# Kernel tuning notes

Measured on AMD Instinct MI355X. Metric: run time of the kernel, lower is better.

The kernel has to match this reference:

```python
import jax, jax.numpy as jnp
from jax import lax
import numpy as np

H = 48; W = 48; C_IN = 256; A_PER = 3
M = A_PER * H * W            # 6912 anchors
IMG = 768.0                  # square image, clip bound for x and y
OBJ_THR = 0.3; IOU_THR = 0.7; TOP_K = 2000
NEG = -1e9                   # finite sentinel for masked scores


def _make_anchors():
    stride = IMG / H
    base = 2.0 * stride
    ratios = np.array([0.5, 1.0, 2.0])
    ws = base * np.sqrt(ratios)          # [3]
    hs = base / np.sqrt(ratios)
    cx = (np.arange(W) + 0.5) * stride
    cy = (np.arange(H) + 0.5) * stride
    cxg, cyg = np.meshgrid(cx, cy)       # [H, W]
    anc = np.stack([
        cxg[None] - ws[:, None, None] / 2,
        cyg[None] - hs[:, None, None] / 2,
        cxg[None] + ws[:, None, None] / 2,
        cyg[None] + hs[:, None, None] / 2,
    ], axis=-1)                           # [3, H, W, 4] matches (anchor, h, w) flatten order
    return jnp.asarray(anc.reshape(-1, 4), jnp.float32)


def setup_inputs() -> dict:
    key = jax.random.key(0)
    ks = jax.random.split(key, 4)
    x = jax.random.normal(ks[0], (1, C_IN, H, W), jnp.float32)
    conv_w = jax.random.normal(ks[1], (256, 256, 3, 3), jnp.float32) * 0.02
    conv_b = jnp.zeros((256,), jnp.float32)
    det_w = jax.random.normal(ks[2], (3, 256, 1, 1), jnp.float32) * 0.02
    det_b = jnp.zeros((3,), jnp.float32)
    reg_w = jax.random.normal(ks[3], (12, 256, 1, 1), jnp.float32) * 0.02
    reg_b = jnp.zeros((12,), jnp.float32)
    anchors = _make_anchors()
    return {"x": x, "conv_w": conv_w, "conv_b": conv_b, "det_w": det_w,
            "det_b": det_b, "reg_w": reg_w, "reg_b": reg_b, "anchors": anchors}


def reference(x, conv_w, conv_b, det_w, det_b, reg_w, reg_b, anchors):
    # ---- FPN 3x3 conv + RPN head (1x1 convs) ----
    inter = lax.conv_general_dilated(
        x, conv_w, (1, 1), 'SAME',
        dimension_numbers=('NCHW', 'OIHW', 'NCHW')) + conv_b[None, :, None, None]
    obj = jax.nn.sigmoid(jnp.einsum('nchw,oc->nohw', inter, det_w[:, :, 0, 0])
                         + det_b[None, :, None, None])          # [1,3,H,W]
    reg = (jnp.einsum('nchw,oc->nohw', inter, reg_w[:, :, 0, 0])
           + reg_b[None, :, None, None])                        # [1,12,H,W]

    scores = obj.reshape(-1)                                    # [M], (anchor,h,w) order
    deltas = reg.reshape(1, 4, A_PER, H, W).transpose(0, 2, 3, 4, 1).reshape(-1, 4)

    # ---- box decode (preserves the source's cx/cy quirk: cx = y1 + w/2, cy = x1 + h/2) ----
    x1, y1, x2, y2 = anchors[:, 0], anchors[:, 1], anchors[:, 2], anchors[:, 3]
    aw = x2 - x1; ah = y2 - y1
    acx = y1 + aw / 2; acy = x1 + ah / 2
    dx, dy, dw, dh = deltas[:, 0], deltas[:, 1], deltas[:, 2], deltas[:, 3]
    px = acx + dx * aw; py = acy + dy * ah
    pw = aw * jnp.exp(dw); ph = ah * jnp.exp(dh)
    boxes = jnp.stack([px - pw / 2, py - ph / 2, px + pw / 2, py + ph / 2], axis=-1)

    # ---- clip to image ----
    boxes = jnp.clip(boxes, 0.0, IMG)

    # ---- validity: degenerate filter (source's naming quirk) + objectness threshold ----
    hts = boxes[:, 2] - boxes[:, 0]
    wds = boxes[:, 3] - boxes[:, 1]
    valid = (hts > 0) & (wds > 0) & (scores > OBJ_THR)

    # ---- greedy NMS (jit-friendly: sort, pairwise IoU, sequential suppression) ----
    s = jnp.where(valid, scores, NEG)
    order = jnp.argsort(-s)
    b = boxes[order]; v = valid[order]; ss = s[order]
    area = (b[:, 2] - b[:, 0]) * (b[:, 3] - b[:, 1])             # [M]
    iw = jnp.clip(jnp.minimum(b[:, None, 2], b[None, :, 2])
                  - jnp.maximum(b[:, None, 0], b[None, :, 0]), 0.0)
    ih = jnp.clip(jnp.minimum(b[:, None, 3], b[None, :, 3])
                  - jnp.maximum(b[:, None, 1], b[None, :, 1]), 0.0)
    inter_a = iw * ih                                             # [M,M]
    iou = inter_a / jnp.maximum(area[:, None] + area[None, :] - inter_a, 1e-9)

    idx = jnp.arange(M)

    def body(suppressed, i):
        keep_i = v[i] & (~suppressed[i])
        sup = keep_i & (iou[i] > IOU_THR) & (idx > i)
        return suppressed | sup, keep_i

    _, keeps = lax.scan(body, jnp.zeros(M, bool), idx)            # keep mask (sorted order)

    # ---- top-k proposal selection (fixed K, padded with sentinels) ----
    out_s = jnp.where(keeps, ss, NEG)
    topv, topi = lax.top_k(out_s, TOP_K)
    vtop = keeps[topi]
    out_scores = jnp.where(vtop, topv, -1.0)                      # [TOP_K]
    out_boxes = jnp.where(vtop[:, None], b[topi], 0.0)            # [TOP_K, 4]
    return out_scores, out_boxes
```

## Files before the change

### kernel.cpp

```cpp
#include <hip/hip_runtime.h>
#include <cstdint>

#define NPX 2304
#define MM 6912
#define NW 108
#define TOPK 2000
#define NEGV -1000000000.0f
#define OBJ_THRF 0.3f
#define IOU_THRF 0.7f
#define IMGF 768.0f
#define KSPLIT 8

typedef unsigned long long u64;
typedef unsigned int u32;

__device__ __forceinline__ u64 shfl64(u64 v, int src) {
  int lo = __shfl((int)(v & 0xffffffffull), src, 64);
  int hi = __shfl((int)(v >> 32), src, 64);
  return ((u64)(u32)hi << 32) | (u32)lo;
}

__global__ __launch_bounds__(256) void k_wt(const float* __restrict__ cw,
                                            float* __restrict__ wt) {
  __shared__ float t[64][65];
  const int it0 = blockIdx.x * 64;
  const int oc0 = blockIdx.y * 64;
  const int tx = threadIdx.x & 63;
  const int ty = threadIdx.x >> 6;
#pragma unroll
  for (int k = 0; k < 16; ++k) {
    int oc = ty + k * 4;
    t[oc][tx] = cw[(oc0 + oc) * 2304 + it0 + tx];
  }
  __syncthreads();
#pragma unroll
  for (int k = 0; k < 16; ++k) {
    int it = ty + k * 4;
    wt[(it0 + it) * 256 + oc0 + tx] = t[tx][it];
  }
}

__global__ __launch_bounds__(256) void k_conv(const float* __restrict__ x,
                                              const float* __restrict__ wt,
                                              float* __restrict__ part) {
  __shared__ float xs[16 * 8 * 52];
  const int tid = threadIdx.x;
  const int px = blockIdx.x * 256 + tid;
  const int oc0 = blockIdx.y * 16;
  const int ks = blockIdx.z;
  const int row = px / 48, col = px % 48;
  const int r0 = (blockIdx.x * 256) / 48;
  const int rbase = row - r0;

  float acc[16];
#pragma unroll
  for (int k = 0; k < 16; ++k) acc[k] = 0.f;

  for (int icc = 0; icc < 2; ++icc) {
    const int ic0 = ks * 32 + icc * 16;
    for (int e = tid; e < 16 * 8 * 50; e += 256) {
      int ic = e / 400, rem = e % 400;
      int r = rem / 50, c = rem % 50 - 1;
      int gr = r0 - 1 + r;
      float v = 0.f;
      if (c >= 0 && c < 48 && gr >= 0 && gr < 48)
        v = x[(ic0 + ic) * NPX + gr * 48 + c];
      xs[(ic * 8 + r) * 52 + (c + 1)] = v;
    }
    __syncthreads();
    for (int ic = 0; ic < 16; ++ic) {
      float xv[9];
#pragma unroll
      for (int dr = 0; dr < 3; ++dr)
#pragma unroll
        for (int dc = 0; dc < 3; ++dc)
          xv[dr * 3 + dc] = xs[(ic * 8 + rbase + dr) * 52 + col + dc];
      const float* wrow = wt + (size_t)(ic0 + ic) * 9 * 256 + oc0;
#pragma unroll
      for (int t = 0; t < 9; ++t) {
        const float* wp = wrow + t * 256;
#pragma unroll
        for (int k = 0; k < 16; ++k) acc[k] += xv[t] * wp[k];
      }
    }
    __syncthreads();
  }
#pragma unroll
  for (int k = 0; k < 16; ++k)
    part[((size_t)ks * 256 + oc0 + k) * NPX + px] = acc[k];
}

__global__ __launch_bounds__(256) void k_decode(const float* __restrict__ part,
                                                const float* __restrict__ cb,
                                                const float* __restrict__ dw,
                                                const float* __restrict__ db,
                                                const float* __restrict__ rw,
                                                const float* __restrict__ rb,
                                                const float* __restrict__ anch,
                                                float* __restrict__ s,
                                                float4* __restrict__ boxes) {
  __shared__ float wl[256 * 16];
  __shared__ float red[4 * 64 * 17];
  const int tid = threadIdx.x;
  const int pxl = tid & 63;
  const int cq = tid >> 6;
  const int px = blockIdx.x * 64 + pxl;
  for (int e = tid; e < 3840; e += 256) {
    int o = e % 15, c = e / 15;
    wl[c * 16 + o] = (o < 3) ? dw[o * 256 + c] : rw[(o - 3) * 256 + c];
  }
  __syncthreads();
  float acc[15];
#pragma unroll
  for (int o = 0; o < 15; o++) acc[o] = 0.f;
  for (int ci = 0; ci < 64; ++ci) {
    int c = cq * 64 + ci;
    float v = cb[c];
#pragma unroll
    for (int kks = 0; kks < KSPLIT; ++kks)
      v += part[((size_t)kks * 256 + c) * NPX + px];
#pragma unroll
    for (int o = 0; o < 15; o++) acc[o] += v * wl[c * 16 + o];
  }
#pragma unroll
  for (int o = 0; o < 15; o++) red[(cq * 64 + pxl) * 17 + o] = acc[o];
  __syncthreads();
  if (tid < 64) {
    const int p = blockIdx.x * 64 + tid;
    float a[15];
#pragma unroll
    for (int o = 0; o < 15; o++)
      a[o] = red[tid * 17 + o] + red[(64 + tid) * 17 + o] +
             red[(128 + tid) * 17 + o] + red[(192 + tid) * 17 + o];
    const float4* an4 = (const float4*)anch;
#pragma unroll
    for (int aa = 0; aa < 3; ++aa) {
      int m = aa * NPX + p;
      float logit = a[aa] + db[aa];
      float score = 1.f / (1.f + expf(-logit));
      float dxv = a[3 + 0 + aa] + rb[0 + aa];
      float dyv = a[3 + 3 + aa] + rb[3 + aa];
      float dwv = a[3 + 6 + aa] + rb[6 + aa];
      float dhv = a[3 + 9 + aa] + rb[9 + aa];
      float4 an = an4[m];
      float aw = an.z - an.x;
      float ah = an.w - an.y;
      float acx = an.y + aw * 0.5f;
      float acy = an.x + ah * 0.5f;
      float pxc = acx + dxv * aw;
      float pyc = acy + dyv * ah;
      float pw = aw * expf(dwv);
      float ph = ah * expf(dhv);
      float b0 = pxc - pw * 0.5f, b1 = pyc - ph * 0.5f;
      float b2 = pxc + pw * 0.5f, b3 = pyc + ph * 0.5f;
      b0 = fminf(fmaxf(b0, 0.f), IMGF);
      b1 = fminf(fmaxf(b1, 0.f), IMGF);
      b2 = fminf(fmaxf(b2, 0.f), IMGF);
      b3 = fminf(fmaxf(b3, 0.f), IMGF);
      float hts = b2 - b0, wds = b3 - b1;
      bool valid = (hts > 0.f) && (wds > 0.f) && (score > OBJ_THRF);
      s[m] = valid ? score : NEGV;
      boxes[m] = make_float4(b0, b1, b2, b3);
    }
  }
}

__global__ __launch_bounds__(256) void k_sortA(const float* __restrict__ s,
                                               u64* __restrict__ keys) {
  __shared__ u64 lds[1024];
  const int tid = threadIdx.x;
  const int b = blockIdx.x;
  for (int v = tid; v < 1024; v += 256) {
    int i = b * 1024 + v;
    u64 p;
    if (i < MM) {
      u32 u = __float_as_uint(s[i]);
      u = u ^ (u32)(((int)u >> 31) | 0x80000000);
      p = ((u64)(~u) << 32) | (u32)i;
    } else {
      p = ~0ull;
    }
    lds[v] = p;
  }
  for (u32 kk = 2; kk <= 1024; kk <<= 1) {
    for (u32 j = kk >> 1; j > 0; j >>= 1) {
      __syncthreads();
#pragma unroll 2
      for (int t = tid; t < 512; t += 256) {
        int i = ((t & ~(j - 1)) << 1) | (t & (j - 1));
        int l = i | j;
        bool up = ((i & kk) == 0);
        u64 a = lds[i], c = lds[l];
        u64 mn = a < c ? a : c;
        u64 mx = a < c ? c : a;
        lds[i] = up ? mn : mx;
        lds[l] = up ? mx : mn;
      }
    }
  }
  __syncthreads();
  for (int v = tid; v < 1024; v += 256) keys[b * 1024 + v] = lds[v];
}

__global__ __launch_bounds__(256) void k_merge(const u64* __restrict__ in,
                                               u64* __restrict__ outk, int L, int fin,
                                               const float* __restrict__ s,
                                               const float4* __restrict__ boxes,
                                               float* __restrict__ ssc,
                                               float4* __restrict__ sboxes) {
  const int i = blockIdx.x * 256 + threadIdx.x;
  const int pair = i / (2 * L);
  const int r = i - pair * 2 * L;
  const u64* A = in + (size_t)pair * 2 * L;
  const u64* B = A + L;
  int lo = (r > L) ? (r - L) : 0;
  int hi = (r < L) ? r : L;
  while (lo < hi) {
    int mid = (lo + hi) >> 1;
    if (A[mid] < B[r - 1 - mid]) lo = mid + 1; else hi = mid;
  }
  int a = lo, bi = r - lo;
  u64 av = (a < L) ? A[a] : ~0ull;
  u64 bv = (bi < L) ? B[bi] : ~0ull;
  u64 o = (av < bv) ? av : bv;
  outk[i] = o;
  if (fin && i < MM) {
    int idx = (int)(u32)o;
    ssc[i] = s[idx];
    sboxes[i] = boxes[idx];
  }
}

__global__ __launch_bounds__(256) void k_zero(u64* __restrict__ nz) {
  int i = blockIdx.x * 256 + threadIdx.x;
  if (i < MM * 2) nz[i] = 0;
}

__global__ __launch_bounds__(256) void k_mask(const float4* __restrict__ sboxes,
                                              u64* __restrict__ mask_t,
                                              u64* __restrict__ nz) {
  __shared__ float4 rb_[64];
  const int rt = blockIdx.x;
  const int w = blockIdx.y * 4 + (threadIdx.x >> 6);
  const int lane = threadIdx.x & 63;
  if (threadIdx.x < 64) rb_[threadIdx.x] = sboxes[rt * 64 + threadIdx.x];
  __syncthreads();
  if (w < rt) return;
  float4 c = sboxes[w * 64 + lane];
  float areaC = (c.z - c.x) * (c.w - c.y);
  u64 myw = 0;
  for (int r = 0; r < 64; ++r) {
    float4 b = rb_[r];
    float iw = fmaxf(fminf(b.z, c.z) - fmaxf(b.x, c.x), 0.f);
    float ih = fmaxf(fminf(b.w, c.w) - fmaxf(b.y, c.y), 0.f);
    float inter = iw * ih;
    float areaB = (b.z - b.x) * (b.w - b.y);
    float un = fmaxf(areaB + areaC - inter, 1e-9f);
    bool bit = (inter / un) > IOU_THRF;
    u64 bal = __ballot(bit);
    if (lane == r) myw = bal;
  }
  mask_t[(size_t)w * MM + rt * 64 + lane] = myw;
  if (myw) atomicOr(&nz[(rt * 64 + lane) * 2 + (w >> 6)], 1ull << (w & 63));
}

__global__ __launch_bounds__(256) void k_scan(const u64* __restrict__ mask_t,
                                              const u64* __restrict__ nz,
                                              const float* __restrict__ ssc,
                                              const float4* __restrict__ sboxes,
                                              float* __restrict__ out) {
  __shared__ u64 remv[NW];
  __shared__ u64 keepw[NW];
  __shared__ int blist[64];
  __shared__ int nkS;
  __shared__ int kcntS;
  __shared__ int pref[NW];
  const int tid = threadIdx.x;
  if (tid < NW) { remv[tid] = 0; keepw[tid] = 0; }
  if (tid == 0) kcntS = 0;
  __syncthreads();

  for (int c = 0; c < NW; ++c) {
    if (tid < 64) {
      const int lane = tid;
      u64 dg = mask_t[(size_t)c * MM + c * 64 + lane];
      float sv = ssc[c * 64 + lane];
      u64 vb = __ballot(sv > OBJ_THRF);
      u64 w0 = remv[c];
      u64 cand = vb & ~w0;
      u64 above = (lane < 63) ? ~((2ull << lane) - 1ull) : 0ull;
      bool inC = ((cand >> lane) & 1ull) != 0;
      u64 conf = __ballot(inC && ((dg & above & cand) != 0ull));
      u64 kb;
      if (conf == 0ull) {
        kb = cand;
      } else {
        u64 w = w0;
        kb = 0;
        u64 rem = cand;
        while (rem) {
          int b = __ffsll(rem) - 1;
          kb |= (1ull << b);
          w |= shfl64(dg, b);
          rem = vb & ~w;
        }
      }
      int below = __popcll(kb & ((1ull << lane) - 1ull));
      if ((kb >> lane) & 1ull) blist[below] = lane;
      if (lane == 0) {
        keepw[c] = kb;
        nkS = __popcll(kb);
        kcntS += __popcll(kb);
      }
    }
    __syncthreads();
    int nk = nkS;
    if (tid < nk) {
      int row = c * 64 + blist[tid];
      u64 nz0 = nz[row * 2], nz1 = nz[row * 2 + 1];
      if (c < 64) {
        nz0 &= (c < 63) ? ~((2ull << c) - 1ull) : 0ull;
      } else {
        nz0 = 0;
        int cc = c - 64;
        nz1 &= ~((2ull << cc) - 1ull);
      }
      while (nz0) {
        int wv = __ffsll(nz0) - 1; nz0 &= nz0 - 1;
        atomicOr(&remv[wv], mask_t[(size_t)wv * MM + row]);
      }
      while (nz1) {
        int wv = __ffsll(nz1) - 1; nz1 &= nz1 - 1;
        atomicOr(&remv[wv + 64], mask_t[(size_t)(wv + 64) * MM + row]);
      }
    }
    __syncthreads();
    if (kcntS >= TOPK) break;
  }

  if (tid == 0) {
    int run = 0;
    for (int cc = 0; cc < NW; ++cc) { pref[cc] = run; run += __popcll(keepw[cc]); }
  }
  __syncthreads();
  for (int e = tid; e < TOPK * 5; e += 256) out[e] = (e < TOPK) ? -1.0f : 0.0f;
  __syncthreads();
  float4* ob = (float4*)(out + TOPK);
  for (int i = tid; i < MM; i += 256) {
    int cc = i >> 6, b = i & 63;
    u64 kb = keepw[cc];
    if ((kb >> b) & 1ull) {
      int rank = pref[cc] + __popcll(kb & ((1ull << b) - 1ull));
      if (rank < TOPK) {
        out[rank] = ssc[i];
        ob[rank] = sboxes[i];
      }
    }
  }
}

extern "C" void kernel_launch(void* const* d_in, const int* in_sizes, int n_in,
                              void* d_out, int out_size, void* d_ws, size_t ws_size,
                              hipStream_t stream) {
  const float* x  = (const float*)d_in[0];
  const float* cw = (const float*)d_in[1];
  const float* cb = (const float*)d_in[2];
  const float* dw = (const float*)d_in[3];
  const float* db = (const float*)d_in[4];
  const float* rw = (const float*)d_in[5];
  const float* rb = (const float*)d_in[6];
  const float* an = (const float*)d_in[7];
  char* ws = (char*)d_ws;
  float*  part   = (float*)(ws);
  u64*    keysA  = (u64*)(ws);
  u64*    keysB  = (u64*)(ws + 65536);
  u64*    mask   = (u64*)(ws);
  u64*    nz     = (u64*)(ws + 5971968);
  float*  wt     = (float*)(ws + 18874368);
  float*  s      = (float*)(ws + 21233664);
  float4* boxes  = (float4*)(ws + 21261312);
  float*  ssc    = (float*)(ws + 21371904);
  float4* sboxes = (float4*)(ws + 21399552);
  float* out = (float*)d_out;

  hipLaunchKernelGGL(k_wt, dim3(36, 4), dim3(256), 0, stream, cw, wt);
  hipLaunchKernelGGL(k_conv, dim3(9, 16, KSPLIT), dim3(256), 0, stream, x, wt, part);
  hipLaunchKernelGGL(k_decode, dim3(36), dim3(256), 0, stream, part, cb, dw, db, rw, rb, an, s, boxes);
  hipLaunchKernelGGL(k_zero, dim3(54), dim3(256), 0, stream, nz);
  hipLaunchKernelGGL(k_sortA, dim3(8), dim3(256), 0, stream, s, keysA);
  hipLaunchKernelGGL(k_merge, dim3(32), dim3(256), 0, stream, keysA, keysB, 1024, 0, s, boxes, ssc, sboxes);
  hipLaunchKernelGGL(k_merge, dim3(32), dim3(256), 0, stream, keysB, keysA, 2048, 0, s, boxes, ssc, sboxes);
  hipLaunchKernelGGL(k_merge, dim3(32), dim3(256), 0, stream, keysA, keysB, 4096, 1, s, boxes, ssc, sboxes);
  hipLaunchKernelGGL(k_mask, dim3(108, 27), dim3(256), 0, stream, sboxes, mask, nz);
  hipLaunchKernelGGL(k_scan, dim3(1), dim3(256), 0, stream, mask, nz, ssc, sboxes, out);
}
```

Baseline: 267.5 us.

## Rework NMS scan as single wavefront, fold nz zeroing into sort, reshape conv grid

The greedy NMS scan now runs as one 64-lane wavefront with no block barriers. Each kept lane ORs its own suppression rows directly, and the next chunk's diagonal mask and scores are prefetched. The separate zeroing kernel is merged into the first sort kernel to save a launch. The conv grid is reordered with 8 output channels per block instead of 16, doubling block count for more parallelism at the cost of more redundant input tile loads.

```diff
diff --git a/kernel.cpp b/kernel.cpp
--- a/kernel.cpp
+++ b/kernel.cpp
@@ -45,16 +45,17 @@
                                               float* __restrict__ part) {
   __shared__ float xs[16 * 8 * 52];
   const int tid = threadIdx.x;
-  const int px = blockIdx.x * 256 + tid;
-  const int oc0 = blockIdx.y * 16;
-  const int ks = blockIdx.z;
+  const int ks = blockIdx.x;
+  const int pxc = blockIdx.y;
+  const int oc0 = blockIdx.z * 8;
+  const int px = pxc * 256 + tid;
   const int row = px / 48, col = px % 48;
-  const int r0 = (blockIdx.x * 256) / 48;
+  const int r0 = (pxc * 256) / 48;
   const int rbase = row - r0;
 
-  float acc[16];
-#pragma unroll
-  for (int k = 0; k < 16; ++k) acc[k] = 0.f;
+  float acc[8];
+#pragma unroll
+  for (int k = 0; k < 8; ++k) acc[k] = 0.f;
 
   for (int icc = 0; icc < 2; ++icc) {
     const int ic0 = ks * 32 + icc * 16;
@@ -80,13 +81,13 @@
       for (int t = 0; t < 9; ++t) {
         const float* wp = wrow + t * 256;
 #pragma unroll
-        for (int k = 0; k < 16; ++k) acc[k] += xv[t] * wp[k];
+        for (int k = 0; k < 8; ++k) acc[k] += xv[t] * wp[k];
       }
     }
     __syncthreads();
   }
 #pragma unroll
-  for (int k = 0; k < 16; ++k)
+  for (int k = 0; k < 8; ++k)
     part[((size_t)ks * 256 + oc0 + k) * NPX + px] = acc[k];
 }
 
@@ -166,10 +167,12 @@
 }
 
 __global__ __launch_bounds__(256) void k_sortA(const float* __restrict__ s,
-                                               u64* __restrict__ keys) {
+                                               u64* __restrict__ keys,
+                                               u64* __restrict__ nz) {
   __shared__ u64 lds[1024];
   const int tid = threadIdx.x;
   const int b = blockIdx.x;
+  for (int i = b * 256 + tid; i < MM * 2; i += 8 * 256) nz[i] = 0;
   for (int v = tid; v < 1024; v += 256) {
     int i = b * 1024 + v;
     u64 p;
@@ -231,11 +234,6 @@
   }
 }
 
-__global__ __launch_bounds__(256) void k_zero(u64* __restrict__ nz) {
-  int i = blockIdx.x * 256 + threadIdx.x;
-  if (i < MM * 2) nz[i] = 0;
-}
-
 __global__ __launch_bounds__(256) void k_mask(const float4* __restrict__ sboxes,
                                               u64* __restrict__ mask_t,
                                               u64* __restrict__ nz) {
@@ -264,89 +262,75 @@
   if (myw) atomicOr(&nz[(rt * 64 + lane) * 2 + (w >> 6)], 1ull << (w & 63));
 }
 
-__global__ __launch_bounds__(256) void k_scan(const u64* __restrict__ mask_t,
-                                              const u64* __restrict__ nz,
-                                              const float* __restrict__ ssc,
-                                              const float4* __restrict__ sboxes,
-                                              float* __restrict__ out) {
+__global__ __launch_bounds__(64) void k_scan(const u64* __restrict__ mask_t,
+                                             const u64* __restrict__ nz,
+                                             const float* __restrict__ ssc,
+                                             const float4* __restrict__ sboxes,
+                                             float* __restrict__ out) {
   __shared__ u64 remv[NW];
   __shared__ u64 keepw[NW];
-  __shared__ int blist[64];
-  __shared__ int nkS;
-  __shared__ int kcntS;
   __shared__ int pref[NW];
-  const int tid = threadIdx.x;
-  if (tid < NW) { remv[tid] = 0; keepw[tid] = 0; }
-  if (tid == 0) kcntS = 0;
-  __syncthreads();
-
+  const int lane = threadIdx.x;
+  for (int i = lane; i < NW; i += 64) { remv[i] = 0; keepw[i] = 0; }
+  int kcnt = 0;
+  u64 dg = mask_t[lane];
+  float sv = ssc[lane];
   for (int c = 0; c < NW; ++c) {
-    if (tid < 64) {
-      const int lane = tid;
-      u64 dg = mask_t[(size_t)c * MM + c * 64 + lane];
-      float sv = ssc[c * 64 + lane];
-      u64 vb = __ballot(sv > OBJ_THRF);
-      u64 w0 = remv[c];
-      u64 cand = vb & ~w0;
-      u64 above = (lane < 63) ? ~((2ull << lane) - 1ull) : 0ull;
-      bool inC = ((cand >> lane) & 1ull) != 0;
-      u64 conf = __ballot(inC && ((dg & above & cand) != 0ull));
-      u64 kb;
-      if (conf == 0ull) {
-        kb = cand;
-      } else {
-        u64 w = w0;
-        kb = 0;
-        u64 rem = cand;
-        while (rem) {
-          int b = __ffsll(rem) - 1;
-          kb |= (1ull << b);
-          w |= shfl64(dg, b);
-          rem = vb & ~w;
-        }
-      }
-      int below = __popcll(kb & ((1ull << lane) - 1ull));
-      if ((kb >> lane) & 1ull) blist[below] = lane;
-      if (lane == 0) {
-        keepw[c] = kb;
-        nkS = __popcll(kb);
-        kcntS += __popcll(kb);
-      }
-    }
-    __syncthreads();
-    int nk = nkS;
-    if (tid < nk) {
-      int row = c * 64 + blist[tid];
-      u64 nz0 = nz[row * 2], nz1 = nz[row * 2 + 1];
+    u64 dg_n = 0; float sv_n = 0.f;
+    if (c + 1 < NW) {
+      dg_n = mask_t[(size_t)(c + 1) * MM + (c + 1) * 64 + lane];
+      sv_n = ssc[(c + 1) * 64 + lane];
+    }
+    u64 vb = __ballot(sv > OBJ_THRF);
+    u64 w0 = remv[c];
+    u64 cand = vb & ~w0;
+    u64 above = (lane < 63) ? ~((2ull << lane) - 1ull) : 0ull;
+    bool inC = ((cand >> lane) & 1ull) != 0;
+    u64 conf = __ballot(inC && ((dg & above & cand) != 0ull));
+    u64 kb;
+    if (conf == 0ull) {
+      kb = cand;
+    } else {
+      u64 w = w0; kb = 0;
+      u64 rem = cand;
+      while (rem) {
+        int b = __ffsll(rem) - 1;
+        kb |= (1ull << b);
+        w |= shfl64(dg, b);
+        rem = vb & ~w;
+      }
+    }
+    if (lane == 0) keepw[c] = kb;
+    if ((kb >> lane) & 1ull) {
+      int rowi = c * 64 + lane;
+      u64 nz0 = nz[rowi * 2], nz1 = nz[rowi * 2 + 1];
       if (c < 64) {
         nz0 &= (c < 63) ? ~((2ull << c) - 1ull) : 0ull;
       } else {
         nz0 = 0;
-        int cc = c - 64;
-        nz1 &= ~((2ull << cc) - 1ull);
+        nz1 &= ~((2ull << (c - 64)) - 1ull);
       }
       while (nz0) {
         int wv = __ffsll(nz0) - 1; nz0 &= nz0 - 1;
-        atomicOr(&remv[wv], mask_t[(size_t)wv * MM + row]);
+        atomicOr(&remv[wv], mask_t[(size_t)wv * MM + rowi]);
       }
       while (nz1) {
         int wv = __ffsll(nz1) - 1; nz1 &= nz1 - 1;
-        atomicOr(&remv[wv + 64], mask_t[(size_t)(wv + 64) * MM + row]);
-      }
-    }
-    __syncthreads();
-    if (kcntS >= TOPK) break;
-  }
-
-  if (tid == 0) {
+        atomicOr(&remv[wv + 64], mask_t[(size_t)(wv + 64) * MM + rowi]);
+      }
+    }
+    kcnt += __popcll(kb);
+    dg = dg_n; sv = sv_n;
+    if (kcnt >= TOPK) break;
+  }
+
+  if (lane == 0) {
     int run = 0;
     for (int cc = 0; cc < NW; ++cc) { pref[cc] = run; run += __popcll(keepw[cc]); }
   }
-  __syncthreads();
-  for (int e = tid; e < TOPK * 5; e += 256) out[e] = (e < TOPK) ? -1.0f : 0.0f;
-  __syncthreads();
+  for (int e = lane; e < TOPK * 5; e += 64) out[e] = (e < TOPK) ? -1.0f : 0.0f;
   float4* ob = (float4*)(out + TOPK);
-  for (int i = tid; i < MM; i += 256) {
+  for (int i = lane; i < MM; i += 64) {
     int cc = i >> 6, b = i & 63;
     u64 kb = keepw[cc];
     if ((kb >> b) & 1ull) {
@@ -384,13 +368,12 @@
   float* out = (float*)d_out;
 
   hipLaunchKernelGGL(k_wt, dim3(36, 4), dim3(256), 0, stream, cw, wt);
-  hipLaunchKernelGGL(k_conv, dim3(9, 16, KSPLIT), dim3(256), 0, stream, x, wt, part);
+  hipLaunchKernelGGL(k_conv, dim3(KSPLIT, 9, 32), dim3(256), 0, stream, x, wt, part);
   hipLaunchKernelGGL(k_decode, dim3(36), dim3(256), 0, stream, part, cb, dw, db, rw, rb, an, s, boxes);
-  hipLaunchKernelGGL(k_zero, dim3(54), dim3(256), 0, stream, nz);
-  hipLaunchKernelGGL(k_sortA, dim3(8), dim3(256), 0, stream, s, keysA);
+  hipLaunchKernelGGL(k_sortA, dim3(8), dim3(256), 0, stream, s, keysA, nz);
   hipLaunchKernelGGL(k_merge, dim3(32), dim3(256), 0, stream, keysA, keysB, 1024, 0, s, boxes, ssc, sboxes);
   hipLaunchKernelGGL(k_merge, dim3(32), dim3(256), 0, stream, keysB, keysA, 2048, 0, s, boxes, ssc, sboxes);
   hipLaunchKernelGGL(k_merge, dim3(32), dim3(256), 0, stream, keysA, keysB, 4096, 1, s, boxes, ssc, sboxes);
   hipLaunchKernelGGL(k_mask, dim3(108, 27), dim3(256), 0, stream, sboxes, mask, nz);
-  hipLaunchKernelGGL(k_scan, dim3(1), dim3(256), 0, stream, mask, nz, ssc, sboxes, out);
-}
+  hipLaunchKernelGGL(k_scan, dim3(1), dim3(64), 0, stream, mask, nz, ssc, sboxes, out);
+}
```

Result: slower. 281.2 us (+5.1%).
